# Kernel optimization log

Hardware: AMD Instinct MI355X
Metric: run time of the kernel (lower is better)

The kernel has to match this reference:

```python
import jax, jax.numpy as jnp
import numpy as np

N = 1_000_000   # total nodes
G = 10_000      # graphs (100 nodes each)
K = 30          # sortpool k = min(30, N//G)
F_IN = 64
LAT = [64, 64, 64, 34]
OUT = 2


def setup_inputs() -> dict:
    key = jax.random.key(0)
    ks = jax.random.split(key, 20)
    s = 0.02
    inp = {
        "x": jax.random.normal(ks[0], (N, F_IN), jnp.float32),
        "edge_index": jax.random.randint(ks[1], (2, 1_000_000), 0, N, dtype=jnp.int32),
        "batch": (jnp.arange(N, dtype=jnp.int32) // (N // G)).astype(jnp.int32),
        # MLP stack params (torch Linear: [out, in])
        "W1": s * jax.random.normal(ks[2], (LAT[0], F_IN), jnp.float32),
        "b1": jnp.zeros((LAT[0],), jnp.float32),
        "W2": s * jax.random.normal(ks[3], (LAT[1], LAT[0]), jnp.float32),
        "b2": jnp.zeros((LAT[1],), jnp.float32),
        "W3": s * jax.random.normal(ks[4], (LAT[2], LAT[1]), jnp.float32),
        "b3": jnp.zeros((LAT[2],), jnp.float32),
        "W4": s * jax.random.normal(ks[5], (LAT[3], LAT[2]), jnp.float32),
        "b4": jnp.zeros((LAT[3],), jnp.float32),
        # Conv1d params (torch: [out_ch, in_ch, kernel])
        "cw1": s * jax.random.normal(ks[6], (16, 1, 5), jnp.float32),
        "cb1": jnp.zeros((16,), jnp.float32),
        "cw2": s * jax.random.normal(ks[7], (32, 16, 5), jnp.float32),
        "cb2": jnp.zeros((32,), jnp.float32),
        # dense head: dense_dim = ((30-2)//2+1 - 5 + 1)*32 = 352
        "Wo": s * jax.random.normal(ks[8], (OUT, 352), jnp.float32),
        "bo": jnp.zeros((OUT,), jnp.float32),
    }
    return inp


def _dgcnn_fwd(x, batch, W1, b1, W2, b2, W3, b3, W4, b4, cw1, cb1, cw2, cb2, Wo, bo):
    # per-node MLP stack
    h = jax.nn.relu(x @ W1.T + b1)
    h = jax.nn.relu(h @ W2.T + b2)
    h = jax.nn.relu(h @ W3.T + b3)
    h = jax.nn.relu(h @ W4.T + b4)  # [N, 34]
    # mean over the FIRST K nodes of each (contiguous, sorted) graph segment
    ones = jnp.ones((h.shape[0],), h.dtype)
    counts = jax.ops.segment_sum(ones, batch, num_segments=G)          # [G]
    starts = jnp.cumsum(counts) - counts                                # segment start offsets
    pos = jnp.arange(h.shape[0], dtype=h.dtype) - starts[batch]         # position within segment
    mask = (pos < K).astype(h.dtype)                                    # first K nodes
    sums = jax.ops.segment_sum(h * mask[:, None], batch, num_segments=G)
    denom = jnp.minimum(counts, jnp.asarray(K, h.dtype))
    pooled = sums / denom[:, None]                                       # [G, 34]
    # conv1d stages (latent_dim[-1]=34 >= 5, so no adaptive pooling branch)
    h = pooled[:, None, :]  # [G, 1, 34]
    dn = ('NCH', 'OIH', 'NCH')
    h = jax.nn.relu(jax.lax.conv_general_dilated(h, cw1, (1,), 'VALID', dimension_numbers=dn) + cb1[None, :, None])  # [G,16,30]
    h = jax.lax.reduce_window(h, -jnp.inf, jax.lax.max, (1, 1, 2), (1, 1, 2), 'VALID')                               # [G,16,15]
    h = jax.nn.relu(jax.lax.conv_general_dilated(h, cw2, (1,), 'VALID', dimension_numbers=dn) + cb2[None, :, None])  # [G,32,11]
    h = h.reshape(h.shape[0], -1)  # [G, 352]
    return h @ Wo.T + bo           # [G, OUT]


def reference(x, edge_index, batch, W1, b1, W2, b2, W3, b3, W4, b4, cw1, cb1, cw2, cb2, Wo, bo):
    # edge_index is accepted but unused by the original forward
    return _dgcnn_fwd(x, batch, W1, b1, W2, b2, W3, b3, W4, b4, cw1, cb1, cw2, cb2, Wo, bo)
```

## Files before the change

kernel.cpp:

```cpp
#include <hip/hip_runtime.h>


#define GRAPHS 10000

__global__ void transpose_cw2_k(const float* __restrict__ cw2, float* __restrict__ cwT) {
  int idx = blockIdx.x * 256 + threadIdx.x;
  if (idx < 2560) {
    int o = idx / 80;
    int r = idx % 80;
    cwT[r * 32 + o] = cw2[idx];
  }
}

__global__ __launch_bounds__(64) void dgcnn_main(
    const float* __restrict__ x,
    const float* __restrict__ W1, const float* __restrict__ b1,
    const float* __restrict__ W2, const float* __restrict__ b2,
    const float* __restrict__ W3, const float* __restrict__ b3,
    const float* __restrict__ W4, const float* __restrict__ b4,
    const float* __restrict__ cw1, const float* __restrict__ cb1,
    const float* __restrict__ cw2t, const float* __restrict__ cw2,
    const float* __restrict__ cb2,
    const float* __restrict__ Wo, const float* __restrict__ bo,
    float* __restrict__ out, int use_t)
{
  __shared__ float act[64][64];
  __shared__ float pooled[2][34];
  __shared__ float mbuf[2][16 * 15];

  const int lane = threadIdx.x;
  const int half = lane >> 5;
  const int pos  = lane & 31;
  const int g    = blockIdx.x * 2 + half;
  const long node = (long)g * 100 + pos;

  float xr[64];
  const float4* xv = (const float4*)(x + node * 64);
  #pragma unroll
  for (int i = 0; i < 16; ++i) {
    float4 v = xv[i];
    xr[4*i+0] = v.x; xr[4*i+1] = v.y; xr[4*i+2] = v.z; xr[4*i+3] = v.w;
  }

  const float* Ws[3] = {W1, W2, W3};
  const float* bs[3] = {b1, b2, b3};
  #pragma unroll
  for (int L = 0; L < 3; ++L) {
    const float* __restrict__ W = Ws[L];
    const float* __restrict__ b = bs[L];
    #pragma unroll 2
    for (int j = 0; j < 64; ++j) {
      const float* __restrict__ wr = W + j * 64;
      float a0 = 0.f, a1 = 0.f, a2 = 0.f, a3 = 0.f;
      #pragma unroll
      for (int k = 0; k < 64; k += 4) {
        a0 += wr[k+0] * xr[k+0];
        a1 += wr[k+1] * xr[k+1];
        a2 += wr[k+2] * xr[k+2];
        a3 += wr[k+3] * xr[k+3];
      }
      float v = (a0 + a1) + (a2 + a3) + b[j];
      act[j][lane] = v > 0.f ? v : 0.f;
    }
    #pragma unroll
    for (int k = 0; k < 64; ++k) xr[k] = act[k][lane];
  }

  const float inv30 = 1.0f / 30.0f;
  #pragma unroll 2
  for (int j = 0; j < 34; ++j) {
    const float* __restrict__ wr = W4 + j * 64;
    float a0 = 0.f, a1 = 0.f, a2 = 0.f, a3 = 0.f;
    #pragma unroll
    for (int k = 0; k < 64; k += 4) {
      a0 += wr[k+0] * xr[k+0];
      a1 += wr[k+1] * xr[k+1];
      a2 += wr[k+2] * xr[k+2];
      a3 += wr[k+3] * xr[k+3];
    }
    float v = (a0 + a1) + (a2 + a3) + b4[j];
    v = v > 0.f ? v : 0.f;
    if (pos >= 30) v = 0.f;
    #pragma unroll
    for (int off = 16; off >= 1; off >>= 1) v += __shfl_xor(v, off);
    if (pos == 0) pooled[half][j] = v * inv30;
  }

  if (lane < 32) {
    int gg = lane >> 4;
    int c  = lane & 15;
    float w0 = cw1[c*5+0], w1 = cw1[c*5+1], w2 = cw1[c*5+2], w3 = cw1[c*5+3], w4 = cw1[c*5+4];
    float bb = cb1[c];
    #pragma unroll
    for (int q = 0; q < 15; ++q) {
      int p = 2 * q;
      float s0 = bb + w0*pooled[gg][p+0] + w1*pooled[gg][p+1] + w2*pooled[gg][p+2]
                    + w3*pooled[gg][p+3] + w4*pooled[gg][p+4];
      float s1 = bb + w0*pooled[gg][p+1] + w1*pooled[gg][p+2] + w2*pooled[gg][p+3]
                    + w3*pooled[gg][p+4] + w4*pooled[gg][p+5];
      float mm = fmaxf(fmaxf(s0, s1), 0.f);
      mbuf[gg][c * 15 + q] = mm;
    }
  }

  const int o = lane & 31;
  const int gg2 = lane >> 5;
  float acc[11];
  float bb2 = cb2[o];
  #pragma unroll
  for (int p = 0; p < 11; ++p) acc[p] = bb2;
  for (int i = 0; i < 16; ++i) {
    float mr[15];
    #pragma unroll
    for (int q = 0; q < 15; ++q) mr[q] = mbuf[gg2][i * 15 + q];
    #pragma unroll
    for (int t = 0; t < 5; ++t) {
      float w = use_t ? cw2t[(i * 5 + t) * 32 + o]
                      : cw2[o * 80 + i * 5 + t];
      #pragma unroll
      for (int p = 0; p < 11; ++p) acc[p] += w * mr[p + t];
    }
  }

  float p0 = 0.f, p1 = 0.f;
  #pragma unroll
  for (int p = 0; p < 11; ++p) {
    float v = acc[p] > 0.f ? acc[p] : 0.f;
    p0 += v * Wo[o * 11 + p];
    p1 += v * Wo[352 + o * 11 + p];
  }
  #pragma unroll
  for (int off = 16; off >= 1; off >>= 1) {
    p0 += __shfl_xor(p0, off);
    p1 += __shfl_xor(p1, off);
  }
  if ((lane & 31) == 0) {
    int gout = blockIdx.x * 2 + half;
    out[gout * 2 + 0] = p0 + bo[0];
    out[gout * 2 + 1] = p1 + bo[1];
  }
}

extern "C" void kernel_launch(void* const* d_in, const int* in_sizes, int n_in,
                              void* d_out, int out_size, void* d_ws, size_t ws_size,
                              hipStream_t stream) {
  const float* x    = (const float*)d_in[0];
  const float* W1   = (const float*)d_in[3];
  const float* b1   = (const float*)d_in[4];
  const float* W2   = (const float*)d_in[5];
  const float* b2   = (const float*)d_in[6];
  const float* W3   = (const float*)d_in[7];
  const float* b3   = (const float*)d_in[8];
  const float* W4   = (const float*)d_in[9];
  const float* b4   = (const float*)d_in[10];
  const float* cw1  = (const float*)d_in[11];
  const float* cb1  = (const float*)d_in[12];
  const float* cw2  = (const float*)d_in[13];
  const float* cb2  = (const float*)d_in[14];
  const float* Wo   = (const float*)d_in[15];
  const float* bo   = (const float*)d_in[16];
  float* out = (float*)d_out;

  float* cwT = (float*)d_ws;
  int use_t = (ws_size >= 2560 * sizeof(float)) ? 1 : 0;
  if (use_t) {
    transpose_cw2_k<<<10, 256, 0, stream>>>(cw2, cwT);
  }
  dgcnn_main<<<GRAPHS / 2, 64, 0, stream>>>(
      x, W1, b1, W2, b2, W3, b3, W4, b4,
      cw1, cb1, cwT, cw2, cb2, Wo, bo, out, use_t);
}
```

Baseline: 859.8 us.

## Use packed float2 FMAs and split activations between registers and LDS

The per-node MLP dot products now use two-wide vector FMAs over packed float2 inputs. Each layer keeps the first 24 outputs in registers and writes the remaining 40 to a smaller per-thread LDS buffer. Pooled and mbuf storage alias that same buffer, guarded by added syncthreads, and launch bounds now request 4 blocks per multiprocessor. The aim is higher occupancy through lower LDS and register use plus higher FMA throughput, at the cost of extra barriers and some rolled loops.

```diff
diff --git a/kernel.cpp b/kernel.cpp
--- a/kernel.cpp
+++ b/kernel.cpp
@@ -1,5 +1,7 @@
 #include <hip/hip_runtime.h>
 
+
+typedef float v2f __attribute__((ext_vector_type(2)));
 
 #define GRAPHS 10000
 
@@ -12,7 +14,24 @@
   }
 }
 
-__global__ __launch_bounds__(64) void dgcnn_main(
+__device__ __forceinline__ float dot64(const float* __restrict__ wr, const v2f (&x)[32]) {
+  const v2f* __restrict__ w2 = (const v2f*)wr;
+  v2f c0 = {0.f, 0.f}, c1 = {0.f, 0.f}, c2 = {0.f, 0.f}, c3 = {0.f, 0.f};
+  #pragma unroll
+  for (int k = 0; k < 32; k += 4) {
+    c0 = __builtin_elementwise_fma(w2[k+0], x[k+0], c0);
+    c1 = __builtin_elementwise_fma(w2[k+1], x[k+1], c1);
+    c2 = __builtin_elementwise_fma(w2[k+2], x[k+2], c2);
+    c3 = __builtin_elementwise_fma(w2[k+3], x[k+3], c3);
+  }
+  v2f s = (c0 + c1) + (c2 + c3);
+  return s.x + s.y;
+}
+
+#define NSTATIC 12
+#define NDYN    20
+
+__global__ __launch_bounds__(64, 4) void dgcnn_main(
     const float* __restrict__ x,
     const float* __restrict__ W1, const float* __restrict__ b1,
     const float* __restrict__ W2, const float* __restrict__ b2,
@@ -24,9 +43,10 @@
     const float* __restrict__ Wo, const float* __restrict__ bo,
     float* __restrict__ out, int use_t)
 {
-  __shared__ float act[64][64];
-  __shared__ float pooled[2][34];
-  __shared__ float mbuf[2][16 * 15];
+  __shared__ v2f smem[64 * 21];
+  v2f (*act)[21] = reinterpret_cast<v2f(*)[21]>(smem);
+  float* pooledB = (float*)smem;
+  float* mbufB   = (float*)smem + 68;
 
   const int lane = threadIdx.x;
   const int half = lane >> 5;
@@ -34,12 +54,13 @@
   const int g    = blockIdx.x * 2 + half;
   const long node = (long)g * 100 + pos;
 
-  float xr[64];
+  v2f xr[32];
   const float4* xv = (const float4*)(x + node * 64);
   #pragma unroll
   for (int i = 0; i < 16; ++i) {
     float4 v = xv[i];
-    xr[4*i+0] = v.x; xr[4*i+1] = v.y; xr[4*i+2] = v.z; xr[4*i+3] = v.w;
+    xr[2*i+0] = (v2f){v.x, v.y};
+    xr[2*i+1] = (v2f){v.z, v.w};
   }
 
   const float* Ws[3] = {W1, W2, W3};
@@ -48,60 +69,57 @@
   for (int L = 0; L < 3; ++L) {
     const float* __restrict__ W = Ws[L];
     const float* __restrict__ b = bs[L];
-    #pragma unroll 2
-    for (int j = 0; j < 64; ++j) {
-      const float* __restrict__ wr = W + j * 64;
-      float a0 = 0.f, a1 = 0.f, a2 = 0.f, a3 = 0.f;
-      #pragma unroll
-      for (int k = 0; k < 64; k += 4) {
-        a0 += wr[k+0] * xr[k+0];
-        a1 += wr[k+1] * xr[k+1];
-        a2 += wr[k+2] * xr[k+2];
-        a3 += wr[k+3] * xr[k+3];
-      }
-      float v = (a0 + a1) + (a2 + a3) + b[j];
-      act[j][lane] = v > 0.f ? v : 0.f;
+
+    v2f yA[NSTATIC];
+    #pragma unroll
+    for (int jp = 0; jp < NSTATIC; ++jp) {
+      float r0 = dot64(W + (2*jp+0)*64, xr) + b[2*jp+0];
+      float r1 = dot64(W + (2*jp+1)*64, xr) + b[2*jp+1];
+      yA[jp] = (v2f){r0 > 0.f ? r0 : 0.f, r1 > 0.f ? r1 : 0.f};
+    }
+    #pragma unroll 1
+    for (int jp = NSTATIC; jp < NSTATIC + NDYN; ++jp) {
+      float r0 = dot64(W + (2*jp+0)*64, xr) + b[2*jp+0];
+      float r1 = dot64(W + (2*jp+1)*64, xr) + b[2*jp+1];
+      act[lane][jp - NSTATIC] = (v2f){r0 > 0.f ? r0 : 0.f, r1 > 0.f ? r1 : 0.f};
     }
     #pragma unroll
-    for (int k = 0; k < 64; ++k) xr[k] = act[k][lane];
+    for (int t = 0; t < NSTATIC; ++t) xr[t] = yA[t];
+    #pragma unroll
+    for (int t = 0; t < NDYN; ++t) xr[NSTATIC + t] = act[lane][t];
   }
 
+  __syncthreads();
+
   const float inv30 = 1.0f / 30.0f;
-  #pragma unroll 2
+  #pragma unroll 1
   for (int j = 0; j < 34; ++j) {
-    const float* __restrict__ wr = W4 + j * 64;
-    float a0 = 0.f, a1 = 0.f, a2 = 0.f, a3 = 0.f;
-    #pragma unroll
-    for (int k = 0; k < 64; k += 4) {
-      a0 += wr[k+0] * xr[k+0];
-      a1 += wr[k+1] * xr[k+1];
-      a2 += wr[k+2] * xr[k+2];
-      a3 += wr[k+3] * xr[k+3];
-    }
-    float v = (a0 + a1) + (a2 + a3) + b4[j];
+    float v = dot64(W4 + j*64, xr) + b4[j];
     v = v > 0.f ? v : 0.f;
     if (pos >= 30) v = 0.f;
     #pragma unroll
     for (int off = 16; off >= 1; off >>= 1) v += __shfl_xor(v, off);
-    if (pos == 0) pooled[half][j] = v * inv30;
+    if (pos == 0) pooledB[half * 34 + j] = v * inv30;
   }
+
+  __syncthreads();
 
   if (lane < 32) {
     int gg = lane >> 4;
     int c  = lane & 15;
+    const float* P = pooledB + gg * 34;
     float w0 = cw1[c*5+0], w1 = cw1[c*5+1], w2 = cw1[c*5+2], w3 = cw1[c*5+3], w4 = cw1[c*5+4];
     float bb = cb1[c];
     #pragma unroll
     for (int q = 0; q < 15; ++q) {
       int p = 2 * q;
-      float s0 = bb + w0*pooled[gg][p+0] + w1*pooled[gg][p+1] + w2*pooled[gg][p+2]
-                    + w3*pooled[gg][p+3] + w4*pooled[gg][p+4];
-      float s1 = bb + w0*pooled[gg][p+1] + w1*pooled[gg][p+2] + w2*pooled[gg][p+3]
-                    + w3*pooled[gg][p+4] + w4*pooled[gg][p+5];
-      float mm = fmaxf(fmaxf(s0, s1), 0.f);
-      mbuf[gg][c * 15 + q] = mm;
+      float s0 = bb + w0*P[p+0] + w1*P[p+1] + w2*P[p+2] + w3*P[p+3] + w4*P[p+4];
+      float s1 = bb + w0*P[p+1] + w1*P[p+2] + w2*P[p+3] + w3*P[p+4] + w4*P[p+5];
+      mbufB[gg * 240 + c * 15 + q] = fmaxf(fmaxf(s0, s1), 0.f);
     }
   }
+
+  __syncthreads();
 
   const int o = lane & 31;
   const int gg2 = lane >> 5;
@@ -109,10 +127,11 @@
   float bb2 = cb2[o];
   #pragma unroll
   for (int p = 0; p < 11; ++p) acc[p] = bb2;
+  #pragma unroll 1
   for (int i = 0; i < 16; ++i) {
     float mr[15];
     #pragma unroll
-    for (int q = 0; q < 15; ++q) mr[q] = mbuf[gg2][i * 15 + q];
+    for (int q = 0; q < 15; ++q) mr[q] = mbufB[gg2 * 240 + i * 15 + q];
     #pragma unroll
     for (int t = 0; t < 5; ++t) {
       float w = use_t ? cw2t[(i * 5 + t) * 32 + o]
```

New measurement: 862.3 us. Within noise of the previous version (+0.3%).
